# Kernel optimization log

Hardware: AMD Instinct MI355X
Metric: run time of the kernel (lower is better)

Reference implementation:

```python
import jax, jax.numpy as jnp
import numpy as np

HEAD_DIM = 64
HIDDEN_SIZE = 3072
NUM_HEADS = 48
B, TXT, VID = 1, 256, 1792
N = TXT + VID


def _layernorm(x, g, b, eps=1e-5):
    mu = jnp.mean(x, axis=-1, keepdims=True)
    xc = x - mu
    var = jnp.mean(xc * xc, axis=-1, keepdims=True)
    return xc * jax.lax.rsqrt(var + eps) * g + b


def _apply_rope1(x, freqs):
    # x: [B, L, H, D]; freqs: [1, 1, Lf, D//2, 2, 2]
    Bx, L, H, D = x.shape
    x_ = x.reshape(Bx, L, H, D // 2, 1, 2)
    # faithful to torch: if dim-2 sizes mismatch (H vs Lf), slice freqs to H
    if x_.shape[2] != 1 and freqs.shape[2] != 1 and x_.shape[2] != freqs.shape[2]:
        freqs = freqs[:, :, : x_.shape[2]]
    out = freqs[..., 0] * x_[..., 0] + freqs[..., 1] * x_[..., 1]
    return out.reshape(Bx, L, H, D).astype(x.dtype)


def setup_inputs() -> dict:
    key = jax.random.key(0)
    ks = jax.random.split(key, 16)
    s = 1.0 / np.sqrt(HIDDEN_SIZE)
    d = dict(
        combined=jax.random.normal(ks[0], (B, N, HIDDEN_SIZE), jnp.float32),
        freqs=jax.random.normal(ks[1], (1, 1, VID, HEAD_DIM // 2, 2, 2), jnp.float32),
        Wq=jax.random.normal(ks[2], (HIDDEN_SIZE, HIDDEN_SIZE), jnp.float32) * s,
        bq=jnp.zeros((HIDDEN_SIZE,), jnp.float32),
        Wk=jax.random.normal(ks[3], (HIDDEN_SIZE, HIDDEN_SIZE), jnp.float32) * s,
        bk=jnp.zeros((HIDDEN_SIZE,), jnp.float32),
        Wv=jax.random.normal(ks[4], (HIDDEN_SIZE, HIDDEN_SIZE), jnp.float32) * s,
        bv=jnp.zeros((HIDDEN_SIZE,), jnp.float32),
        Wo=jax.random.normal(ks[5], (HIDDEN_SIZE, HIDDEN_SIZE), jnp.float32) * s,
        bo=jnp.zeros((HIDDEN_SIZE,), jnp.float32),
        gq=jnp.ones((HEAD_DIM,), jnp.float32),
        bgq=jnp.zeros((HEAD_DIM,), jnp.float32),
        gk=jnp.ones((HEAD_DIM,), jnp.float32),
        bgk=jnp.zeros((HEAD_DIM,), jnp.float32),
        txt_len=TXT,
    )
    return d


def reference(combined, freqs, Wq, bq, Wk, bk, Wv, bv, Wo, bo, gq, bgq, gk, bgk, txt_len):
    Bx, Nx, _ = combined.shape
    Q = (combined @ Wq.T + bq).reshape(Bx, Nx, NUM_HEADS, HEAD_DIM)
    K = (combined @ Wk.T + bk).reshape(Bx, Nx, NUM_HEADS, HEAD_DIM)
    V = (combined @ Wv.T + bv).reshape(Bx, Nx, NUM_HEADS, HEAD_DIM)
    Q = _layernorm(Q, gq, bgq)
    K = _layernorm(K, gk, bgk)
    if freqs is not None and Nx - txt_len > 0:
        Q_vid = _apply_rope1(Q[:, txt_len:], freqs)
        K_vid = _apply_rope1(K[:, txt_len:], freqs)
        Q = jnp.concatenate([Q[:, :txt_len], Q_vid], axis=1)
        K = jnp.concatenate([K[:, :txt_len], K_vid], axis=1)
    # SDPA in fp32: [B, H, N, D]
    q = Q.transpose(0, 2, 1, 3).astype(jnp.float32)
    k = K.transpose(0, 2, 1, 3).astype(jnp.float32)
    v = V.transpose(0, 2, 1, 3).astype(jnp.float32)
    scale = 1.0 / np.sqrt(HEAD_DIM)
    scores = jnp.einsum('bhqd,bhkd->bhqk', q, k) * scale
    probs = jax.nn.softmax(scores, axis=-1)
    attn = jnp.einsum('bhqk,bhkd->bhqd', probs, v).astype(combined.dtype)
    attn = attn.transpose(0, 2, 1, 3).reshape(Bx, Nx, HIDDEN_SIZE)
    out = attn @ Wo.T + bo
    return out[:, txt_len:], out[:, :txt_len]
```

## Files before the change

kernel.cpp:

```cpp
#include <hip/hip_runtime.h>
#include <hip/hip_bf16.h>

typedef __attribute__((ext_vector_type(8))) short bf16x8;
typedef __attribute__((ext_vector_type(4))) float f32x4;
typedef unsigned int __attribute__((address_space(1))) as1_uint;
typedef unsigned int __attribute__((address_space(3))) as3_uint;

#define TXT 256
#define VIDN 1792
#define SEQ 2048
#define HID 3072
#define NH 48
#define HD 64
#define QSCALE 0.18033688011112042f

__device__ __forceinline__ unsigned short f2bf(float f) {
  union { float f; unsigned int u; } x; x.f = f;
  unsigned int r = x.u + 0x7fffu + ((x.u >> 16) & 1u);
  return (unsigned short)(r >> 16);
}

__device__ __forceinline__ void gload16(const void* g, void* l) {
  __builtin_amdgcn_global_load_lds((const as1_uint*)g, (as3_uint*)l, 16, 0, 0);
}

__global__ __launch_bounds__(256) void cvt_kernel(const float* __restrict__ s,
                                                  unsigned short* __restrict__ d, int n) {
  int i = (blockIdx.x * 256 + threadIdx.x) * 4;
  if (i >= n) return;
  float4 v = *(const float4*)(s + i);
  ushort4 o;
  o.x = f2bf(v.x); o.y = f2bf(v.y); o.z = f2bf(v.z); o.w = f2bf(v.w);
  *(ushort4*)(d + i) = o;
}

template<int MODE>
__global__ __launch_bounds__(256) void gemm_bt(
    const unsigned short* __restrict__ A,
    const unsigned short* __restrict__ Bt,
    int K, int ntn,
    float* __restrict__ Cq, unsigned short* __restrict__ VtOut, const float* __restrict__ bv,
    float* __restrict__ Cout, const float* __restrict__ bo)
{
  __shared__ unsigned short la[128 * 32];
  __shared__ unsigned short lb[128 * 32];
  const int tid = threadIdx.x;
  const int mt = blockIdx.x / ntn, nt = blockIdx.x % ntn;
  const int m0 = mt * 128, n0 = nt * 128;
  const int w = tid >> 6, lane = tid & 63, lr = lane & 15, lg = lane >> 4;
  const int wm = (w >> 1) * 64, wn = (w & 1) * 64;
  f32x4 acc[4][4] = {};
  for (int k0 = 0; k0 < K; k0 += 32) {
#pragma unroll
    for (int c = 0; c < 2; ++c) {
      int off = (c * 256 + tid) * 16;
      int row = off >> 6, cb = off & 63;
      gload16(A + (size_t)(m0 + row) * K + k0 + (cb >> 1), (char*)la + off);
      gload16(Bt + (size_t)(n0 + row) * K + k0 + (cb >> 1), (char*)lb + off);
    }
    __syncthreads();
    bf16x8 af[4], bfr[4];
#pragma unroll
    for (int f = 0; f < 4; ++f) {
      af[f]  = *(const bf16x8*)&la[(wm + f * 16 + lr) * 32 + lg * 8];
      bfr[f] = *(const bf16x8*)&lb[(wn + f * 16 + lr) * 32 + lg * 8];
    }
#pragma unroll
    for (int mf = 0; mf < 4; ++mf)
#pragma unroll
      for (int nf = 0; nf < 4; ++nf)
        acc[mf][nf] = __builtin_amdgcn_mfma_f32_16x16x32_bf16(af[mf], bfr[nf], acc[mf][nf], 0, 0, 0);
    __syncthreads();
  }

  if (MODE == 0) {
    if (n0 < 6144) {
#pragma unroll
      for (int mf = 0; mf < 4; ++mf)
#pragma unroll
        for (int nf = 0; nf < 4; ++nf) {
          int row = m0 + wm + mf * 16 + lg * 4;
          int col = n0 + wn + nf * 16 + lr;
#pragma unroll
          for (int j = 0; j < 4; ++j)
            Cq[(size_t)(row + j) * 6144 + col] = acc[mf][nf][j];
        }
    } else {
#pragma unroll
      for (int mf = 0; mf < 4; ++mf)
#pragma unroll
        for (int nf = 0; nf < 4; ++nf) {
          int srow = m0 + wm + mf * 16 + lg * 4;
          int n2 = n0 - 6144 + wn + nf * 16 + lr;
          float b = bv[n2];
          ushort4 pk;
          pk.x = f2bf(acc[mf][nf][0] + b);
          pk.y = f2bf(acc[mf][nf][1] + b);
          pk.z = f2bf(acc[mf][nf][2] + b);
          pk.w = f2bf(acc[mf][nf][3] + b);
          *(ushort4*)(VtOut + (size_t)n2 * SEQ + srow) = pk;
        }
    }
  } else {
#pragma unroll
    for (int mf = 0; mf < 4; ++mf)
#pragma unroll
      for (int nf = 0; nf < 4; ++nf) {
        int row = m0 + wm + mf * 16 + lg * 4;
        int col = n0 + wn + nf * 16 + lr;
        float b = bo[col];
#pragma unroll
        for (int j = 0; j < 4; ++j) {
          int s = row + j;
          int orow = (s >= TXT) ? (s - TXT) : (VIDN + s);
          Cout[(size_t)orow * HID + col] = acc[mf][nf][j] + b;
        }
      }
  }
}

__global__ __launch_bounds__(256) void ln_rope_kernel(
    const float* __restrict__ QK,
    const float* __restrict__ bq, const float* __restrict__ bk,
    const float* __restrict__ gq, const float* __restrict__ bgq,
    const float* __restrict__ gk, const float* __restrict__ bgk,
    const float* __restrict__ freqs,
    unsigned short* __restrict__ Qh, unsigned short* __restrict__ Kh)
{
  int wid = blockIdx.x * 4 + (threadIdx.x >> 6);
  int lane = threadIdx.x & 63;
  int s = wid / 96;
  int rem = wid - s * 96;
  int h = rem >> 1, qk = rem & 1;
  int col = h * 64 + lane;
  float x = QK[(size_t)s * 6144 + qk * 3072 + col] + (qk ? bk[col] : bq[col]);
  float m = x;
#pragma unroll
  for (int msk = 1; msk < 64; msk <<= 1) m += __shfl_xor(m, msk);
  float mu = m * (1.0f / 64.0f);
  float xc = x - mu;
  float v = xc * xc;
#pragma unroll
  for (int msk = 1; msk < 64; msk <<= 1) v += __shfl_xor(v, msk);
  float rstd = rsqrtf(v * (1.0f / 64.0f) + 1e-5f);
  float y = xc * rstd * (qk ? gk[lane] : gq[lane]) + (qk ? bgk[lane] : bgq[lane]);
  if (s >= TXT) {
    float p = __shfl_xor(y, 1);
    float xe = (lane & 1) ? p : y;
    float xo = (lane & 1) ? y : p;
    int base = h * 128 + (lane >> 1) * 4 + (lane & 1) * 2;
    y = freqs[base] * xe + freqs[base + 1] * xo;
  }
  if (!qk) y *= QSCALE;
  (qk ? Kh : Qh)[((size_t)h * SEQ + s) * 64 + lane] = f2bf(y);
}

__global__ __launch_bounds__(256) void fattn_kernel(
    const unsigned short* __restrict__ Qh, const unsigned short* __restrict__ Kh,
    const unsigned short* __restrict__ Vt, unsigned short* __restrict__ ctx)
{
  __shared__ unsigned short kt[2][64][32];
  __shared__ unsigned short vt[2][64][32];
  __shared__ unsigned short pl[4][16][72];
  const int h = blockIdx.x >> 5;
  const int q0 = (blockIdx.x & 31) * 64;
  const int tid = threadIdx.x, w = tid >> 6, lane = tid & 63, lr = lane & 15, lg = lane >> 4;

  bf16x8 qf0, qf1;
  {
    const unsigned short* qp = Qh + ((size_t)h * SEQ + q0 + w * 16 + lr) * 64 + lg * 8;
    qf0 = *(const bf16x8*)qp;
    qf1 = *(const bf16x8*)(qp + 32);
  }
  f32x4 oacc[4] = {};
  float mrun = -1e30f, lrun = 0.f;

  for (int kv0 = 0; kv0 < SEQ; kv0 += 64) {
    __syncthreads();
#pragma unroll
    for (int c = 0; c < 2; ++c) {
      int off = (c * 256 + tid) * 16;
      int half = off >> 12;
      int rem = off & 4095;
      int row = rem >> 6, cb = rem & 63;
      gload16(Kh + ((size_t)h * SEQ + kv0 + row) * 64 + half * 32 + (cb >> 1), (char*)kt + off);
      gload16(Vt + ((size_t)(h * 64 + row)) * SEQ + kv0 + half * 32 + (cb >> 1), (char*)vt + off);
    }
    __syncthreads();

    f32x4 sacc[4] = {};
    __builtin_amdgcn_s_setprio(1);
#pragma unroll
    for (int nf = 0; nf < 4; ++nf) {
      bf16x8 a0 = *(const bf16x8*)&kt[0][nf * 16 + lr][lg * 8];
      bf16x8 a1 = *(const bf16x8*)&kt[1][nf * 16 + lr][lg * 8];
      sacc[nf] = __builtin_amdgcn_mfma_f32_16x16x32_bf16(a0, qf0, sacc[nf], 0, 0, 0);
      sacc[nf] = __builtin_amdgcn_mfma_f32_16x16x32_bf16(a1, qf1, sacc[nf], 0, 0, 0);
    }
    __builtin_amdgcn_s_setprio(0);

    float mx;
    {
      float t0 = fmaxf(fmaxf(sacc[0][0], sacc[0][1]), fmaxf(sacc[0][2], sacc[0][3]));
      float t1 = fmaxf(fmaxf(sacc[1][0], sacc[1][1]), fmaxf(sacc[1][2], sacc[1][3]));
      float t2 = fmaxf(fmaxf(sacc[2][0], sacc[2][1]), fmaxf(sacc[2][2], sacc[2][3]));
      float t3 = fmaxf(fmaxf(sacc[3][0], sacc[3][1]), fmaxf(sacc[3][2], sacc[3][3]));
      mx = fmaxf(fmaxf(t0, t1), fmaxf(t2, t3));
    }
    mx = fmaxf(mx, __shfl_xor(mx, 16));
    mx = fmaxf(mx, __shfl_xor(mx, 32));

    if (!__all(mx <= mrun + 8.0f)) {
      float mn = fmaxf(mrun, mx);
      float corr = exp2f(mrun - mn);
      lrun *= corr;
      mrun = mn;
      float c0 = __shfl(corr, lg * 4 + 0);
      float c1 = __shfl(corr, lg * 4 + 1);
      float c2 = __shfl(corr, lg * 4 + 2);
      float c3 = __shfl(corr, lg * 4 + 3);
#pragma unroll
      for (int df = 0; df < 4; ++df) {
        oacc[df][0] *= c0; oacc[df][1] *= c1;
        oacc[df][2] *= c2; oacc[df][3] *= c3;
      }
    }

    float pr[4][4];
#pragma unroll
    for (int nf = 0; nf < 4; ++nf)
#pragma unroll
      for (int r = 0; r < 4; ++r)
        pr[nf][r] = exp2f(sacc[nf][r] - mrun);
    float rs;
    {
      float s0 = (pr[0][0] + pr[0][1]) + (pr[0][2] + pr[0][3]);
      float s1 = (pr[1][0] + pr[1][1]) + (pr[1][2] + pr[1][3]);
      float s2 = (pr[2][0] + pr[2][1]) + (pr[2][2] + pr[2][3]);
      float s3 = (pr[3][0] + pr[3][1]) + (pr[3][2] + pr[3][3]);
      rs = (s0 + s1) + (s2 + s3);
    }
    rs += __shfl_xor(rs, 16);
    rs += __shfl_xor(rs, 32);
    lrun += rs;

#pragma unroll
    for (int nf = 0; nf < 4; ++nf) {
      union { __hip_bfloat162 h; unsigned int u; } c0, c1;
      c0.h = __float22bfloat162_rn(make_float2(pr[nf][0], pr[nf][1]));
      c1.h = __float22bfloat162_rn(make_float2(pr[nf][2], pr[nf][3]));
      uint2 pw; pw.x = c0.u; pw.y = c1.u;
      *(uint2*)&pl[w][lr][nf * 16 + lg * 4] = pw;
    }

    bf16x8 pa0 = *(const bf16x8*)&pl[w][lr][lg * 8];
    bf16x8 pa1 = *(const bf16x8*)&pl[w][lr][32 + lg * 8];
    __builtin_amdgcn_s_setprio(1);
#pragma unroll
    for (int df = 0; df < 4; ++df) {
      bf16x8 v0 = *(const bf16x8*)&vt[0][df * 16 + lr][lg * 8];
      bf16x8 v1 = *(const bf16x8*)&vt[1][df * 16 + lr][lg * 8];
      oacc[df] = __builtin_amdgcn_mfma_f32_16x16x32_bf16(pa0, v0, oacc[df], 0, 0, 0);
      oacc[df] = __builtin_amdgcn_mfma_f32_16x16x32_bf16(pa1, v1, oacc[df], 0, 0, 0);
    }
    __builtin_amdgcn_s_setprio(0);
  }

  float linv = 1.0f / lrun;
  float i0 = __shfl(linv, lg * 4 + 0);
  float i1 = __shfl(linv, lg * 4 + 1);
  float i2 = __shfl(linv, lg * 4 + 2);
  float i3 = __shfl(linv, lg * 4 + 3);
#pragma unroll
  for (int df = 0; df < 4; ++df) {
    int s = q0 + w * 16 + lg * 4;
    int dcol = h * 64 + df * 16 + lr;
    ctx[(size_t)(s + 0) * HID + dcol] = f2bf(oacc[df][0] * i0);
    ctx[(size_t)(s + 1) * HID + dcol] = f2bf(oacc[df][1] * i1);
    ctx[(size_t)(s + 2) * HID + dcol] = f2bf(oacc[df][2] * i2);
    ctx[(size_t)(s + 3) * HID + dcol] = f2bf(oacc[df][3] * i3);
  }
}

extern "C" void kernel_launch(void* const* d_in, const int* in_sizes, int n_in,
                              void* d_out, int out_size, void* d_ws, size_t ws_size,
                              hipStream_t stream) {
  const float* combined = (const float*)d_in[0];
  const float* freqs    = (const float*)d_in[1];
  const float* Wq  = (const float*)d_in[2];
  const float* bq  = (const float*)d_in[3];
  const float* Wk  = (const float*)d_in[4];
  const float* bk  = (const float*)d_in[5];
  const float* Wv  = (const float*)d_in[6];
  const float* bv  = (const float*)d_in[7];
  const float* Wo  = (const float*)d_in[8];
  const float* bo  = (const float*)d_in[9];
  const float* gq  = (const float*)d_in[10];
  const float* bgq = (const float*)d_in[11];
  const float* gk  = (const float*)d_in[12];
  const float* bgk = (const float*)d_in[13];
  float* out = (float*)d_out;

  char* ws = (char*)d_ws;
  unsigned short* Abf  = (unsigned short*)ws; ws += (size_t)SEQ * HID * 2;
  unsigned short* Wqkv = (unsigned short*)ws; ws += (size_t)3 * HID * HID * 2;
  float*          QK   = (float*)ws;          ws += (size_t)SEQ * 6144 * 4;
  unsigned short* Qh   = (unsigned short*)ws; ws += (size_t)NH * SEQ * HD * 2;
  unsigned short* Kh   = (unsigned short*)ws; ws += (size_t)NH * SEQ * HD * 2;
  unsigned short* Vt   = (unsigned short*)ws; ws += (size_t)NH * HD * SEQ * 2;
  unsigned short* Wob  = (unsigned short*)QK;
  unsigned short* ctx  = Abf;

  cvt_kernel<<<(SEQ * HID) / 1024, 256, 0, stream>>>(combined, Abf, SEQ * HID);
  cvt_kernel<<<(HID * HID) / 1024, 256, 0, stream>>>(Wq, Wqkv, HID * HID);
  cvt_kernel<<<(HID * HID) / 1024, 256, 0, stream>>>(Wk, Wqkv + (size_t)HID * HID, HID * HID);
  cvt_kernel<<<(HID * HID) / 1024, 256, 0, stream>>>(Wv, Wqkv + (size_t)2 * HID * HID, HID * HID);

  gemm_bt<0><<<16 * 72, 256, 0, stream>>>(Abf, Wqkv, HID, 72, QK, Vt, bv, nullptr, nullptr);

  ln_rope_kernel<<<(SEQ * NH * 2) / 4, 256, 0, stream>>>(QK, bq, bk, gq, bgq, gk, bgk, freqs, Qh, Kh);

  cvt_kernel<<<(HID * HID) / 1024, 256, 0, stream>>>(Wo, Wob, HID * HID);

  fattn_kernel<<<NH * 32, 256, 0, stream>>>(Qh, Kh, Vt, ctx);

  gemm_bt<1><<<16 * 24, 256, 0, stream>>>(ctx, Wob, HID, 24, nullptr, nullptr, nullptr, out, bo);
}
```

Before: 469.4 us.

## Use 256x256 four-stage pipelined GEMM, 128-query attention blocks, fused weight conversion

```diff
diff --git a/kernel.cpp b/kernel.cpp
--- a/kernel.cpp
+++ b/kernel.cpp
@@ -34,80 +34,130 @@
   *(ushort4*)(d + i) = o;
 }
 
+__global__ __launch_bounds__(256) void cvt3_kernel(const float* __restrict__ a,
+                                                   const float* __restrict__ b,
+                                                   const float* __restrict__ c,
+                                                   unsigned short* __restrict__ d) {
+  const int per = (HID * HID) / 1024;
+  int bid = blockIdx.x;
+  int m = bid / per, r = bid - m * per;
+  const float* s = (m == 0) ? a : (m == 1) ? b : c;
+  int i = (r * 256 + threadIdx.x) * 4;
+  float4 v = *(const float4*)(s + i);
+  ushort4 o;
+  o.x = f2bf(v.x); o.y = f2bf(v.y); o.z = f2bf(v.z); o.w = f2bf(v.w);
+  *(ushort4*)(d + (size_t)m * HID * HID + i) = o;
+}
+
 template<int MODE>
-__global__ __launch_bounds__(256) void gemm_bt(
+__global__ __launch_bounds__(512) void gemm256(
     const unsigned short* __restrict__ A,
     const unsigned short* __restrict__ Bt,
     int K, int ntn,
-    float* __restrict__ Cq, unsigned short* __restrict__ VtOut, const float* __restrict__ bv,
+    float* __restrict__ Cq, unsigned short* __restrict__ Vt, const float* __restrict__ bv,
     float* __restrict__ Cout, const float* __restrict__ bo)
 {
-  __shared__ unsigned short la[128 * 32];
-  __shared__ unsigned short lb[128 * 32];
+  __shared__ unsigned short lds[4 * 2 * 8192];
   const int tid = threadIdx.x;
   const int mt = blockIdx.x / ntn, nt = blockIdx.x % ntn;
-  const int m0 = mt * 128, n0 = nt * 128;
+  const int m0 = mt * 256, n0 = nt * 256;
   const int w = tid >> 6, lane = tid & 63, lr = lane & 15, lg = lane >> 4;
-  const int wm = (w >> 1) * 64, wn = (w & 1) * 64;
-  f32x4 acc[4][4] = {};
-  for (int k0 = 0; k0 < K; k0 += 32) {
-#pragma unroll
-    for (int c = 0; c < 2; ++c) {
-      int off = (c * 256 + tid) * 16;
-      int row = off >> 6, cb = off & 63;
-      gload16(A + (size_t)(m0 + row) * K + k0 + (cb >> 1), (char*)la + off);
-      gload16(Bt + (size_t)(n0 + row) * K + k0 + (cb >> 1), (char*)lb + off);
-    }
-    __syncthreads();
-    bf16x8 af[4], bfr[4];
-#pragma unroll
-    for (int f = 0; f < 4; ++f) {
-      af[f]  = *(const bf16x8*)&la[(wm + f * 16 + lr) * 32 + lg * 8];
-      bfr[f] = *(const bf16x8*)&lb[(wn + f * 16 + lr) * 32 + lg * 8];
-    }
-#pragma unroll
-    for (int mf = 0; mf < 4; ++mf)
-#pragma unroll
-      for (int nf = 0; nf < 4; ++nf)
-        acc[mf][nf] = __builtin_amdgcn_mfma_f32_16x16x32_bf16(af[mf], bfr[nf], acc[mf][nf], 0, 0, 0);
-    __syncthreads();
-  }
+  const int wr = w >> 2, wc = w & 3;
+  f32x4 acc[8][4] = {};
+  const int NT = K >> 5;
+
+#define STAGE(t)                                                               \
+  {                                                                            \
+    const int slot_ = (t) & 3;                                                 \
+    const int k0_ = (t) << 5;                                                  \
+    _Pragma("unroll")                                                          \
+    for (int c = 0; c < 2; ++c) {                                              \
+      int off = (c * 512 + tid) * 16;                                          \
+      int row = off >> 6, cb = off & 63;                                       \
+      gload16(A + (size_t)(m0 + row) * K + k0_ + (cb >> 1),                    \
+              (char*)lds + slot_ * 32768 + off);                               \
+      gload16(Bt + (size_t)(n0 + row) * K + k0_ + (cb >> 1),                   \
+              (char*)lds + slot_ * 32768 + 16384 + off);                       \
+    }                                                                          \
+  }
+
+#define COMPUTE(t)                                                             \
+  {                                                                            \
+    const unsigned short* lA = lds + ((t) & 3) * 16384;                        \
+    const unsigned short* lB = lA + 8192;                                      \
+    bf16x8 bfr[4];                                                             \
+    _Pragma("unroll")                                                          \
+    for (int nf = 0; nf < 4; ++nf)                                             \
+      bfr[nf] = *(const bf16x8*)&lB[(wc * 64 + nf * 16 + lr) * 32 + lg * 8];   \
+    __builtin_amdgcn_s_setprio(1);                                             \
+    _Pragma("unroll")                                                          \
+    for (int mf = 0; mf < 8; ++mf) {                                           \
+      bf16x8 af = *(const bf16x8*)&lA[(wr * 128 + mf * 16 + lr) * 32 + lg * 8];\
+      acc[mf][0] = __builtin_amdgcn_mfma_f32_16x16x32_bf16(af, bfr[0], acc[mf][0], 0, 0, 0); \
+      acc[mf][1] = __builtin_amdgcn_mfma_f32_16x16x32_bf16(af, bfr[1], acc[mf][1], 0, 0, 0); \
+      acc[mf][2] = __builtin_amdgcn_mfma_f32_16x16x32_bf16(af, bfr[2], acc[mf][2], 0, 0, 0); \
+      acc[mf][3] = __builtin_amdgcn_mfma_f32_16x16x32_bf16(af, bfr[3], acc[mf][3], 0, 0, 0); \
+    }                                                                          \
+    __builtin_amdgcn_s_setprio(0);                                             \
+  }
+
+  STAGE(0); STAGE(1); STAGE(2);
+  int t = 0;
+  for (; t < NT - 3; ++t) {
+    __builtin_amdgcn_s_barrier();
+    STAGE(t + 3);
+    asm volatile("s_waitcnt vmcnt(12)" ::: "memory");
+    COMPUTE(t);
+  }
+  __builtin_amdgcn_s_barrier();
+  asm volatile("s_waitcnt vmcnt(8)" ::: "memory");
+  COMPUTE(t); ++t;
+  __builtin_amdgcn_s_barrier();
+  asm volatile("s_waitcnt vmcnt(4)" ::: "memory");
+  COMPUTE(t); ++t;
+  __builtin_amdgcn_s_barrier();
+  asm volatile("s_waitcnt vmcnt(0)" ::: "memory");
+  COMPUTE(t);
+#undef STAGE
+#undef COMPUTE
 
   if (MODE == 0) {
     if (n0 < 6144) {
 #pragma unroll
-      for (int mf = 0; mf < 4; ++mf)
+      for (int mf = 0; mf < 8; ++mf) {
+        int row = m0 + wr * 128 + mf * 16 + lg * 4;
 #pragma unroll
         for (int nf = 0; nf < 4; ++nf) {
-          int row = m0 + wm + mf * 16 + lg * 4;
-          int col = n0 + wn + nf * 16 + lr;
+          int col = n0 + wc * 64 + nf * 16 + lr;
 #pragma unroll
           for (int j = 0; j < 4; ++j)
             Cq[(size_t)(row + j) * 6144 + col] = acc[mf][nf][j];
         }
+      }
     } else {
 #pragma unroll
-      for (int mf = 0; mf < 4; ++mf)
+      for (int mf = 0; mf < 8; ++mf) {
+        int srow = m0 + wr * 128 + mf * 16 + lg * 4;
 #pragma unroll
         for (int nf = 0; nf < 4; ++nf) {
-          int srow = m0 + wm + mf * 16 + lg * 4;
-          int n2 = n0 - 6144 + wn + nf * 16 + lr;
+          int n2 = n0 - 6144 + wc * 64 + nf * 16 + lr;
           float b = bv[n2];
           ushort4 pk;
           pk.x = f2bf(acc[mf][nf][0] + b);
           pk.y = f2bf(acc[mf][nf][1] + b);
           pk.z = f2bf(acc[mf][nf][2] + b);
           pk.w = f2bf(acc[mf][nf][3] + b);
-          *(ushort4*)(VtOut + (size_t)n2 * SEQ + srow) = pk;
+          *(ushort4*)(Vt + (size_t)n2 * SEQ + srow) = pk;
         }
+      }
     }
   } else {
 #pragma unroll
-    for (int mf = 0; mf < 4; ++mf)
+    for (int mf = 0; mf < 8; ++mf) {
+      int row = m0 + wr * 128 + mf * 16 + lg * 4;
 #pragma unroll
       for (int nf = 0; nf < 4; ++nf) {
-        int row = m0 + wm + mf * 16 + lg * 4;
-        int col = n0 + wn + nf * 16 + lr;
+        int col = n0 + wc * 64 + nf * 16 + lr;
         float b = bo[col];
 #pragma unroll
         for (int j = 0; j < 4; ++j) {
@@ -116,6 +166,7 @@
           Cout[(size_t)orow * HID + col] = acc[mf][nf][j] + b;
         }
       }
+    }
   }
 }
 
@@ -155,15 +206,15 @@
   (qk ? Kh : Qh)[((size_t)h * SEQ + s) * 64 + lane] = f2bf(y);
 }
 
-__global__ __launch_bounds__(256) void fattn_kernel(
+__global__ __launch_bounds__(512) void fattn_kernel(
     const unsigned short* __restrict__ Qh, const unsigned short* __restrict__ Kh,
     const unsigned short* __restrict__ Vt, unsigned short* __restrict__ ctx)
 {
   __shared__ unsigned short kt[2][64][32];
   __shared__ unsigned short vt[2][64][32];
-  __shared__ unsigned short pl[4][16][72];
-  const int h = blockIdx.x >> 5;
-  const int q0 = (blockIdx.x & 31) * 64;
+  __shared__ unsigned short pl[8][16][72];
+  const int h = blockIdx.x >> 4;
+  const int q0 = (blockIdx.x & 15) * 128;
   const int tid = threadIdx.x, w = tid >> 6, lane = tid & 63, lr = lane & 15, lg = lane >> 4;
 
   bf16x8 qf0, qf1;
@@ -177,9 +228,8 @@
 
   for (int kv0 = 0; kv0 < SEQ; kv0 += 64) {
     __syncthreads();
-#pragma unroll
-    for (int c = 0; c < 2; ++c) {
-      int off = (c * 256 + tid) * 16;
+    {
+      int off = tid * 16;
       int half = off >> 12;
       int rem = off & 4095;
       int row = rem >> 6, cb = rem & 63;
@@ -312,17 +362,15 @@
   unsigned short* ctx  = Abf;
 
   cvt_kernel<<<(SEQ * HID) / 1024, 256, 0, stream>>>(combined, Abf, SEQ * HID);
-  cvt_kernel<<<(HID * HID) / 1024, 256, 0, stream>>>(Wq, Wqkv, HID * HID);
-  cvt_kernel<<<(HID * HID) / 1024, 256, 0, stream>>>(Wk, Wqkv + (size_t)HID * HID, HID * HID);
-  cvt_kernel<<<(HID * HID) / 1024, 256, 0, stream>>>(Wv, Wqkv + (size_t)2 * HID * HID, HID * HID);
-
-  gemm_bt<0><<<16 * 72, 256, 0, stream>>>(Abf, Wqkv, HID, 72, QK, Vt, bv, nullptr, nullptr);
+  cvt3_kernel<<<3 * (HID * HID) / 1024, 256, 0, stream>>>(Wq, Wk, Wv, Wqkv);
+
+  gemm256<0><<<8 * 36, 512, 0, stream>>>(Abf, Wqkv, HID, 36, QK, Vt, bv, nullptr, nullptr);
 
   ln_rope_kernel<<<(SEQ * NH * 2) / 4, 256, 0, stream>>>(QK, bq, bk, gq, bgq, gk, bgk, freqs, Qh, Kh);
 
   cvt_kernel<<<(HID * HID) / 1024, 256, 0, stream>>>(Wo, Wob, HID * HID);
 
-  fattn_kernel<<<NH * 32, 256, 0, stream>>>(Qh, Kh, Vt, ctx);
-
-  gemm_bt<1><<<16 * 24, 256, 0, stream>>>(ctx, Wob, HID, 24, nullptr, nullptr, nullptr, out, bo);
-}
+  fattn_kernel<<<NH * 16, 512, 0, stream>>>(Qh, Kh, Vt, ctx);
+
+  gemm256<1><<<8 * 12, 512, 0, stream>>>(ctx, Wob, HID, 12, nullptr, nullptr, nullptr, out, bo);
+}
```

Result: faster. 453.7 us (-3.3%).
